# Optimization experiments

Measured on AMD Instinct MI355X. Metric: run time of the kernel, lower is better.

The kernel has to match this reference:

```python
import jax, jax.numpy as jnp
import numpy as np

D = 192  # volume side
B = 3    # batch fixed by default weight length

def setup_inputs() -> dict:
    key = jax.random.key(0)
    k1, k2 = jax.random.split(key)
    pred = jax.random.normal(k1, (B, 1, D, D, D), dtype=jnp.float32)
    target = jax.random.uniform(k2, (B, 1, D, D, D), dtype=jnp.float32)
    weight = jnp.ones((B,), dtype=jnp.float32)
    return {"pred": pred, "target": target, "weight": weight}

def reference(pred, target, weight):
    smooth = jnp.float32(1.0)
    size = pred.shape[0]
    p = jax.nn.sigmoid(pred).reshape(size, -1)   # [B, N]
    t = target.reshape(size, -1)                 # [B, N]
    # weight[i] is a scalar per sample, so it multiplies each reduction term
    inter = jnp.sum(p * t, axis=1) * weight      # [B]
    psum = jnp.sum(p, axis=1) * weight           # [B]
    tsum = jnp.sum(t, axis=1) * weight           # [B]
    dice = (2.0 * inter + smooth) / (psum + tsum + smooth)
    return jnp.sum(1.0 - dice) / size
```

## Files before the change

kernel.cpp:

```cpp
#include <hip/hip_runtime.h>


constexpr int B_BATCH  = 3;
constexpr int D3       = 192 * 192 * 192;
constexpr int N4       = D3 / 4;
constexpr int BLK      = 256;
constexpr int ITERS    = 12;
constexpr int BLOCKS_X = N4 / (BLK * ITERS);

__device__ __forceinline__ float fsigmoid(float x) {
    return __builtin_amdgcn_rcpf(1.f + __expf(-x));
}

__global__ __launch_bounds__(BLK) void dice_partial(
    const float* __restrict__ pred,
    const float* __restrict__ target,
    float* __restrict__ part )
{
    const int b = blockIdx.y;
    const float4* __restrict__ p4 =
        reinterpret_cast<const float4*>(pred) + (size_t)b * N4;
    const float4* __restrict__ t4 =
        reinterpret_cast<const float4*>(target) + (size_t)b * N4;

    const int base = blockIdx.x * (BLK * ITERS) + threadIdx.x;

    float sp[4]  = {0.f, 0.f, 0.f, 0.f};
    float st[4]  = {0.f, 0.f, 0.f, 0.f};
    float spt[4] = {0.f, 0.f, 0.f, 0.f};

    #pragma unroll
    for (int j = 0; j < ITERS; ++j) {
        float4 pv = p4[base + j * BLK];
        float4 tv = t4[base + j * BLK];
        float s0 = fsigmoid(pv.x);
        float s1 = fsigmoid(pv.y);
        float s2 = fsigmoid(pv.z);
        float s3 = fsigmoid(pv.w);
        const int a = j & 3;
        sp[a]  += (s0 + s1) + (s2 + s3);
        st[a]  += (tv.x + tv.y) + (tv.z + tv.w);
        spt[a] += (s0 * tv.x + s1 * tv.y) + (s2 * tv.z + s3 * tv.w);
    }

    float rsp  = (sp[0]  + sp[1])  + (sp[2]  + sp[3]);
    float rst  = (st[0]  + st[1])  + (st[2]  + st[3]);
    float rspt = (spt[0] + spt[1]) + (spt[2] + spt[3]);

    #pragma unroll
    for (int off = 32; off > 0; off >>= 1) {
        rsp  += __shfl_down(rsp,  off);
        rst  += __shfl_down(rst,  off);
        rspt += __shfl_down(rspt, off);
    }

    __shared__ float red[4][3];
    const int wave = threadIdx.x >> 6;
    const int lane = threadIdx.x & 63;
    if (lane == 0) {
        red[wave][0] = rsp;
        red[wave][1] = rst;
        red[wave][2] = rspt;
    }
    __syncthreads();
    if (threadIdx.x == 0) {
        float a0 = (red[0][0] + red[1][0]) + (red[2][0] + red[3][0]);
        float a1 = (red[0][1] + red[1][1]) + (red[2][1] + red[3][1]);
        float a2 = (red[0][2] + red[1][2]) + (red[2][2] + red[3][2]);
        float* o = part + ((size_t)b * BLOCKS_X + blockIdx.x) * 3;
        o[0] = a0;
        o[1] = a1;
        o[2] = a2;
    }
}

__global__ __launch_bounds__(576) void dice_final(
    const float* __restrict__ part ,
    const float* __restrict__ weight,
    float* __restrict__ out)
{
    __shared__ float sums[9];
    const int w    = threadIdx.x >> 6;
    const int lane = threadIdx.x & 63;
    const int b = w / 3;
    const int c = w % 3;

    float s = 0.f;
    #pragma unroll
    for (int i = 0; i < BLOCKS_X / 64; ++i)
        s += part[((size_t)b * BLOCKS_X + i * 64 + lane) * 3 + c];
    #pragma unroll
    for (int off = 32; off > 0; off >>= 1)
        s += __shfl_down(s, off);
    if (lane == 0) sums[w] = s;
    __syncthreads();

    if (threadIdx.x == 0) {
        float loss = 0.f;
        #pragma unroll
        for (int bb = 0; bb < B_BATCH; ++bb) {
            float wgt = weight[bb];
            float sp  = sums[bb * 3 + 0];
            float stv = sums[bb * 3 + 1];
            float spt = sums[bb * 3 + 2];
            float dice = (2.f * spt * wgt + 1.f) / ((sp + stv) * wgt + 1.f);
            loss += 1.f - dice;
        }
        out[0] = loss / (float)B_BATCH;
    }
}

extern "C" void kernel_launch(void* const* d_in, const int* in_sizes, int n_in,
                              void* d_out, int out_size, void* d_ws, size_t ws_size,
                              hipStream_t stream) {
    const float* pred   = (const float*)d_in[0];
    const float* target = (const float*)d_in[1];
    const float* weight = (const float*)d_in[2];
    float* out  = (float*)d_out;
    float* part = (float*)d_ws;

    dim3 grid(BLOCKS_X, B_BATCH);
    dice_partial<<<grid, BLK, 0, stream>>>(pred, target, part);
    dice_final<<<1, 576, 0, stream>>>(part, weight, out);
}
```

Before: 31.74 us.

## Fuse final reduction into partial kernel via atomics and last-block ticket

Replaces the two-kernel reduction with a single kernel. Each block atomically adds its three partial sums into padded global accumulators, then takes a ticket, and the last block computes the dice loss. This removes the second kernel launch and the partials round trip, but adds a memset launch and global atomic contention across about 2000 blocks. Float atomics also make the summation order nondeterministic.

```diff
diff --git a/kernel.cpp b/kernel.cpp
--- a/kernel.cpp
+++ b/kernel.cpp
@@ -7,15 +7,19 @@
 constexpr int BLK      = 256;
 constexpr int ITERS    = 12;
 constexpr int BLOCKS_X = N4 / (BLK * ITERS);
+constexpr int GRID     = BLOCKS_X * B_BATCH;
 
 __device__ __forceinline__ float fsigmoid(float x) {
     return __builtin_amdgcn_rcpf(1.f + __expf(-x));
 }
 
-__global__ __launch_bounds__(BLK) void dice_partial(
+__global__ __launch_bounds__(BLK) void dice_fused(
     const float* __restrict__ pred,
     const float* __restrict__ target,
-    float* __restrict__ part )
+    const float* __restrict__ weight,
+    float* __restrict__ out,
+    int* __restrict__ ticket,
+    float* __restrict__ sums )
 {
     const int b = blockIdx.y;
     const float4* __restrict__ p4 =
@@ -55,6 +59,7 @@
     }
 
     __shared__ float red[4][3];
+    __shared__ int is_last;
     const int wave = threadIdx.x >> 6;
     const int lane = threadIdx.x & 63;
     if (lane == 0) {
@@ -63,47 +68,35 @@
         red[wave][2] = rspt;
     }
     __syncthreads();
+
     if (threadIdx.x == 0) {
         float a0 = (red[0][0] + red[1][0]) + (red[2][0] + red[3][0]);
         float a1 = (red[0][1] + red[1][1]) + (red[2][1] + red[3][1]);
         float a2 = (red[0][2] + red[1][2]) + (red[2][2] + red[3][2]);
-        float* o = part + ((size_t)b * BLOCKS_X + blockIdx.x) * 3;
-        o[0] = a0;
-        o[1] = a1;
-        o[2] = a2;
+        float o0 = atomicAdd(&sums[(b * 3 + 0) * 16], a0);
+        float o1 = atomicAdd(&sums[(b * 3 + 1) * 16], a1);
+        float o2 = atomicAdd(&sums[(b * 3 + 2) * 16], a2);
+        asm volatile("" :: "v"(o0), "v"(o1), "v"(o2));
+        int prev = __hip_atomic_fetch_add(ticket, 1, __ATOMIC_ACQ_REL,
+                                          __HIP_MEMORY_SCOPE_AGENT);
+        is_last = (prev == GRID - 1);
     }
-}
-
-__global__ __launch_bounds__(576) void dice_final(
-    const float* __restrict__ part ,
-    const float* __restrict__ weight,
-    float* __restrict__ out)
-{
-    __shared__ float sums[9];
-    const int w    = threadIdx.x >> 6;
-    const int lane = threadIdx.x & 63;
-    const int b = w / 3;
-    const int c = w % 3;
-
-    float s = 0.f;
-    #pragma unroll
-    for (int i = 0; i < BLOCKS_X / 64; ++i)
-        s += part[((size_t)b * BLOCKS_X + i * 64 + lane) * 3 + c];
-    #pragma unroll
-    for (int off = 32; off > 0; off >>= 1)
-        s += __shfl_down(s, off);
-    if (lane == 0) sums[w] = s;
     __syncthreads();
+    if (!is_last) return;
 
     if (threadIdx.x == 0) {
+        float tot[9];
+        #pragma unroll
+        for (int c9 = 0; c9 < 9; ++c9)
+            tot[c9] = atomicAdd(&sums[c9 * 16], 0.0f);
         float loss = 0.f;
         #pragma unroll
         for (int bb = 0; bb < B_BATCH; ++bb) {
-            float wgt = weight[bb];
-            float sp  = sums[bb * 3 + 0];
-            float stv = sums[bb * 3 + 1];
-            float spt = sums[bb * 3 + 2];
-            float dice = (2.f * spt * wgt + 1.f) / ((sp + stv) * wgt + 1.f);
+            float wgt  = weight[bb];
+            float ssp  = tot[bb * 3 + 0];
+            float sst  = tot[bb * 3 + 1];
+            float sspt = tot[bb * 3 + 2];
+            float dice = (2.f * sspt * wgt + 1.f) / ((ssp + sst) * wgt + 1.f);
             loss += 1.f - dice;
         }
         out[0] = loss / (float)B_BATCH;
@@ -116,10 +109,12 @@
     const float* pred   = (const float*)d_in[0];
     const float* target = (const float*)d_in[1];
     const float* weight = (const float*)d_in[2];
-    float* out  = (float*)d_out;
-    float* part = (float*)d_ws;
+    float* out    = (float*)d_out;
+    int*   ticket = (int*)d_ws;
+    float* sums   = (float*)((char*)d_ws + 64);
+
+    hipMemsetAsync(d_ws, 0, 640, stream);
 
     dim3 grid(BLOCKS_X, B_BATCH);
-    dice_partial<<<grid, BLK, 0, stream>>>(pred, target, part);
-    dice_final<<<1, 576, 0, stream>>>(part, weight, out);
+    dice_fused<<<grid, BLK, 0, stream>>>(pred, target, weight, out, ticket, sums);
 }
```

Result: slower. 88.20 us (+177.9%).

## Batch loads in groups, shrink per-block work, and transpose partials layout

Applied to the files above, without the earlier changes.

Drops per-thread iterations from 12 to 8 and issues loads in groups of four (all pred loads, then all target loads) before computing, so more memory requests are in flight per thread. The grid therefore grows to 864 blocks per batch. Partial sums are stored as a struct-of-arrays so the final kernel reads them with coalesced, strided loops across 4 waves instead of 9. The trade-offs are more blocks and partials to reduce, plus higher register pressure from the grouped loads.

```diff
diff --git a/kernel.cpp b/kernel.cpp
--- a/kernel.cpp
+++ b/kernel.cpp
@@ -5,7 +5,8 @@
 constexpr int D3       = 192 * 192 * 192;
 constexpr int N4       = D3 / 4;
 constexpr int BLK      = 256;
-constexpr int ITERS    = 12;
+constexpr int ITERS    = 8;
+constexpr int GROUP    = 4;
 constexpr int BLOCKS_X = N4 / (BLK * ITERS);
 
 __device__ __forceinline__ float fsigmoid(float x) {
@@ -25,22 +26,29 @@
 
     const int base = blockIdx.x * (BLK * ITERS) + threadIdx.x;
 
-    float sp[4]  = {0.f, 0.f, 0.f, 0.f};
-    float st[4]  = {0.f, 0.f, 0.f, 0.f};
-    float spt[4] = {0.f, 0.f, 0.f, 0.f};
+    float sp[GROUP]  = {0.f, 0.f, 0.f, 0.f};
+    float st[GROUP]  = {0.f, 0.f, 0.f, 0.f};
+    float spt[GROUP] = {0.f, 0.f, 0.f, 0.f};
 
     #pragma unroll
-    for (int j = 0; j < ITERS; ++j) {
-        float4 pv = p4[base + j * BLK];
-        float4 tv = t4[base + j * BLK];
-        float s0 = fsigmoid(pv.x);
-        float s1 = fsigmoid(pv.y);
-        float s2 = fsigmoid(pv.z);
-        float s3 = fsigmoid(pv.w);
-        const int a = j & 3;
-        sp[a]  += (s0 + s1) + (s2 + s3);
-        st[a]  += (tv.x + tv.y) + (tv.z + tv.w);
-        spt[a] += (s0 * tv.x + s1 * tv.y) + (s2 * tv.z + s3 * tv.w);
+    for (int g = 0; g < ITERS / GROUP; ++g) {
+        float4 pv[GROUP], tv[GROUP];
+        #pragma unroll
+        for (int k = 0; k < GROUP; ++k)
+            pv[k] = p4[base + (g * GROUP + k) * BLK];
+        #pragma unroll
+        for (int k = 0; k < GROUP; ++k)
+            tv[k] = t4[base + (g * GROUP + k) * BLK];
+        #pragma unroll
+        for (int k = 0; k < GROUP; ++k) {
+            float s0 = fsigmoid(pv[k].x);
+            float s1 = fsigmoid(pv[k].y);
+            float s2 = fsigmoid(pv[k].z);
+            float s3 = fsigmoid(pv[k].w);
+            sp[k]  += (s0 + s1) + (s2 + s3);
+            st[k]  += (tv[k].x + tv[k].y) + (tv[k].z + tv[k].w);
+            spt[k] += (s0 * tv[k].x + s1 * tv[k].y) + (s2 * tv[k].z + s3 * tv[k].w);
+        }
     }
 
     float rsp  = (sp[0]  + sp[1])  + (sp[2]  + sp[3]);
@@ -67,43 +75,41 @@
         float a0 = (red[0][0] + red[1][0]) + (red[2][0] + red[3][0]);
         float a1 = (red[0][1] + red[1][1]) + (red[2][1] + red[3][1]);
         float a2 = (red[0][2] + red[1][2]) + (red[2][2] + red[3][2]);
-        float* o = part + ((size_t)b * BLOCKS_X + blockIdx.x) * 3;
-        o[0] = a0;
-        o[1] = a1;
-        o[2] = a2;
+        part[(b * 3 + 0) * BLOCKS_X + blockIdx.x] = a0;
+        part[(b * 3 + 1) * BLOCKS_X + blockIdx.x] = a1;
+        part[(b * 3 + 2) * BLOCKS_X + blockIdx.x] = a2;
     }
 }
 
-__global__ __launch_bounds__(576) void dice_final(
+__global__ __launch_bounds__(256) void dice_final(
     const float* __restrict__ part ,
     const float* __restrict__ weight,
     float* __restrict__ out)
 {
     __shared__ float sums[9];
-    const int w    = threadIdx.x >> 6;
+    const int wave = threadIdx.x >> 6;
     const int lane = threadIdx.x & 63;
-    const int b = w / 3;
-    const int c = w % 3;
 
-    float s = 0.f;
-    #pragma unroll
-    for (int i = 0; i < BLOCKS_X / 64; ++i)
-        s += part[((size_t)b * BLOCKS_X + i * 64 + lane) * 3 + c];
-    #pragma unroll
-    for (int off = 32; off > 0; off >>= 1)
-        s += __shfl_down(s, off);
-    if (lane == 0) sums[w] = s;
+    for (int c9 = wave; c9 < 9; c9 += 4) {
+        float s = 0.f;
+        for (int i = lane; i < BLOCKS_X; i += 64)
+            s += part[c9 * BLOCKS_X + i];
+        #pragma unroll
+        for (int off = 32; off > 0; off >>= 1)
+            s += __shfl_down(s, off);
+        if (lane == 0) sums[c9] = s;
+    }
     __syncthreads();
 
     if (threadIdx.x == 0) {
         float loss = 0.f;
         #pragma unroll
         for (int bb = 0; bb < B_BATCH; ++bb) {
-            float wgt = weight[bb];
-            float sp  = sums[bb * 3 + 0];
-            float stv = sums[bb * 3 + 1];
-            float spt = sums[bb * 3 + 2];
-            float dice = (2.f * spt * wgt + 1.f) / ((sp + stv) * wgt + 1.f);
+            float wgt  = weight[bb];
+            float ssp  = sums[bb * 3 + 0];
+            float sst  = sums[bb * 3 + 1];
+            float sspt = sums[bb * 3 + 2];
+            float dice = (2.f * sspt * wgt + 1.f) / ((ssp + sst) * wgt + 1.f);
             loss += 1.f - dice;
         }
         out[0] = loss / (float)B_BATCH;
@@ -121,5 +127,5 @@
 
     dim3 grid(BLOCKS_X, B_BATCH);
     dice_partial<<<grid, BLK, 0, stream>>>(pred, target, part);
-    dice_final<<<1, 576, 0, stream>>>(part, weight, out);
+    dice_final<<<1, 256, 0, stream>>>(part, weight, out);
 }
```

After: 43.71 us. +37.7%, slower.
